# Kernel tuning notes

Measured on AMD Instinct MI355X. Metric: run time of the kernel, lower is better.

## Reference

```python
import jax, jax.numpy as jnp
import numpy as np

B, T, C = 4, 2048, 1024
H, G = 16, 4            # n_head, n_groups (GQA)
D = C // H              # head_dim = 64
NEG_INF = -1e30


def setup_inputs() -> dict:
    key = jax.random.key(0)
    k1, k2, k3, k4 = jax.random.split(key, 4)
    x = jax.random.normal(k1, (B, T, C), dtype=jnp.float32)
    Wq = jax.random.normal(k2, (C, C), dtype=jnp.float32) * 0.02
    Wkv = jax.random.normal(k3, (2 * G * D, C), dtype=jnp.float32) * 0.02
    Wproj = jax.random.normal(k4, (C, C), dtype=jnp.float32) * 0.02
    b_proj = jnp.zeros((C,), dtype=jnp.float32)
    return {"x": x, "Wq": Wq, "Wkv": Wkv, "Wproj": Wproj, "b_proj": b_proj}


def reference(x, Wq, Wkv, Wproj, b_proj):
    # q projection: [B,T,C] -> [B,H,T,D]
    q = (x @ Wq.T).reshape(B, T, H, D).transpose(0, 2, 1, 3)
    # fused kv projection -> split into k,v each [B,G,T,D]
    kv = x @ Wkv.T
    k = kv[..., : G * D].reshape(B, T, G, D).transpose(0, 2, 1, 3)
    v = kv[..., G * D :].reshape(B, T, G, D).transpose(0, 2, 1, 3)
    # torch .repeat tiles groups: head h uses kv group h % G
    k = jnp.tile(k, (1, H // G, 1, 1))  # [B,H,T,D]
    v = jnp.tile(v, (1, H // G, 1, 1))
    scale = 1.0 / jnp.sqrt(jnp.asarray(D, dtype=x.dtype))
    scores = jnp.einsum("bhqd,bhkd->bhqk", q, k) * scale  # [B,H,T,T]
    causal = jnp.tril(jnp.ones((T, T), dtype=bool))
    scores = jnp.where(causal, scores, NEG_INF)
    att = jax.nn.softmax(scores, axis=-1)
    y = jnp.einsum("bhqk,bhkd->bhqd", att, v)  # [B,H,T,D]
    y = y.transpose(0, 2, 1, 3).reshape(B, T, C)
    return y @ Wproj.T + b_proj
```

## Files before the change

### kernel.cpp

```cpp
#include <hip/hip_runtime.h>
#include <math.h>
#include <stdint.h>

#define B_ 4
#define T_ 2048
#define C_ 1024
#define H_ 16
#define G_ 4
#define D_ 64
#define KVC_ 512

typedef unsigned short u16;
typedef short bf16x8 __attribute__((ext_vector_type(8)));
typedef float f32x4 __attribute__((ext_vector_type(4)));

__device__ __forceinline__ u16 f2bf(float f) {
  uint32_t u = __builtin_bit_cast(uint32_t, f);
  u += 0x7fffu + ((u >> 16) & 1u);
  return (u16)(u >> 16);
}

__device__ __forceinline__ void gload16(const void* g, void* l) {
  __builtin_amdgcn_global_load_lds((const __attribute__((address_space(1))) void*)g,
                                   (__attribute__((address_space(3))) void*)l, 16, 0, 0);
}

__global__ __launch_bounds__(256)
void cvt_bf16(const float* __restrict__ s, u16* __restrict__ d, int n4, float scale) {
  int i = blockIdx.x * 256 + threadIdx.x;
  const int stride = gridDim.x * 256;
  for (; i < n4; i += stride) {
    const float4 v = ((const float4*)s)[i];
    uint2 o;
    o.x = (uint32_t)f2bf(v.x * scale) | ((uint32_t)f2bf(v.y * scale) << 16);
    o.y = (uint32_t)f2bf(v.z * scale) | ((uint32_t)f2bf(v.w * scale) << 16);
    ((uint2*)d)[i] = o;
  }
}

template <int OUTF32>
__global__ __launch_bounds__(256)
void gemm_bf16(const u16* __restrict__ A, const u16* __restrict__ W,
               const float* __restrict__ bias, void* __restrict__ outp,
               int N, int K) {
  __shared__ __align__(16) u16 As[128 * 32];
  __shared__ __align__(16) u16 Ws[128 * 32];
  const int tid = threadIdx.x;
  const int l = tid & 63, w = tid >> 6;
  const int lhi = l >> 4, llo = l & 15;
  const int wr = w >> 1, wc = w & 1;
  const int m0 = blockIdx.x * 128, n0 = blockIdx.y * 128;

  const u16* a_src = A + (size_t)(m0 + 32 * w + (l >> 2)) * K + 8 * (l & 3);
  const u16* w_src = W + (size_t)(n0 + 32 * w + (l >> 2)) * K + 8 * (l & 3);
  u16* asl = As + 1024 * w;
  u16* wsl = Ws + 1024 * w;

  const f32x4 zero4 = {0.f, 0.f, 0.f, 0.f};
  f32x4 acc[4][4];
#pragma unroll
  for (int i = 0; i < 4; ++i)
#pragma unroll
    for (int j = 0; j < 4; ++j) acc[i][j] = zero4;

  for (int k0 = 0; k0 < K; k0 += 32) {
    __syncthreads();
    gload16(a_src + k0, asl);
    gload16(a_src + k0 + 16 * K, asl + 512);
    gload16(w_src + k0, wsl);
    gload16(w_src + k0 + 16 * K, wsl + 512);
    __syncthreads();
    bf16x8 af[4], wf[4];
#pragma unroll
    for (int mt = 0; mt < 4; ++mt)
      af[mt] = *(const bf16x8*)(As + (wr * 64 + mt * 16 + llo) * 32 + lhi * 8);
#pragma unroll
    for (int nt = 0; nt < 4; ++nt)
      wf[nt] = *(const bf16x8*)(Ws + (wc * 64 + nt * 16 + llo) * 32 + lhi * 8);
#pragma unroll
    for (int mt = 0; mt < 4; ++mt)
#pragma unroll
      for (int nt = 0; nt < 4; ++nt)
        acc[mt][nt] = __builtin_amdgcn_mfma_f32_16x16x32_bf16(af[mt], wf[nt], acc[mt][nt], 0, 0, 0);
  }

#pragma unroll
  for (int mt = 0; mt < 4; ++mt)
#pragma unroll
    for (int nt = 0; nt < 4; ++nt)
#pragma unroll
      for (int r = 0; r < 4; ++r) {
        const int row = m0 + wr * 64 + mt * 16 + 4 * lhi + r;
        const int col = n0 + wc * 64 + nt * 16 + llo;
        if (OUTF32)
          ((float*)outp)[(size_t)row * N + col] = acc[mt][nt][r] + bias[col];
        else
          ((u16*)outp)[(size_t)row * N + col] = f2bf(acc[mt][nt][r]);
      }
}

__global__ __launch_bounds__(256)
void attn_kernel(const u16* __restrict__ Qb, const u16* __restrict__ KVb,
                 u16* __restrict__ Yb) {
  const int qt = blockIdx.x;
  const int bh = blockIdx.y;
  const int b = bh >> 4, h = bh & 15, g = h & (G_ - 1);
  const int tid = threadIdx.x;
  const int l = tid & 63, w = tid >> 6;
  const int lhi = l >> 4, llo = l & 15, l7 = l & 7;

  __shared__ __align__(16) u16 Ks[64 * 64];
  __shared__ __align__(16) u16 Vt[64 * 64];
  __shared__ __align__(16) u16 Ps[4][16 * 64];

  const int q0 = qt * 64;
  const int qrow = q0 + 16 * w + llo;
  const u16* qptr = Qb + (size_t)(b * T_ + qrow) * C_ + h * D_ + 8 * lhi;
  const bf16x8 qf0 = *(const bf16x8*)(qptr);
  const bf16x8 qf1 = *(const bf16x8*)(qptr + 32);

  const f32x4 zero4 = {0.f, 0.f, 0.f, 0.f};
  f32x4 o[4];
#pragma unroll
  for (int i = 0; i < 4; ++i) o[i] = zero4;
  float m_s = -__builtin_inff();
  float l_s = 0.f;

  const int vkr = 2 * (tid >> 3);
  const int vdc = tid & 7;
  const int kr0s = 16 * w + (l >> 3);
  const int kcs = (l & 7);
  u16* ksl = Ks + 1024 * w;
  u16* Pw = Ps[w];
  const int rbase = 4 * lhi;

  for (int kt = 0; kt <= qt; ++kt) {
    const int kv0 = b * T_ + kt * 64;
    const u16* vsrc = KVb + (size_t)(kv0 + vkr) * KVC_ + G_ * D_ + g * D_ + 8 * vdc;
    const uint4 v0 = *(const uint4*)vsrc;
    const uint4 v1 = *(const uint4*)(vsrc + KVC_);

    __syncthreads();
    {
      const u16* ks0 = KVb + (size_t)(kv0 + kr0s) * KVC_ + g * D_ + 8 * (kcs ^ (kr0s & 7));
      gload16(ks0, ksl);
      gload16(ks0 + 8 * KVC_, ksl + 512);
    }
    {
      const u16* pv0 = (const u16*)&v0;
      const u16* pv1 = (const u16*)&v1;
#pragma unroll
      for (int i = 0; i < 8; ++i) {
        const int d = 8 * vdc + i;
        const uint32_t val = (uint32_t)pv0[i] | ((uint32_t)pv1[i] << 16);
        const int byte = d * 128 + (((vkr >> 3) ^ (d & 7)) << 4) + (vkr & 7) * 2;
        *(uint32_t*)((char*)Vt + byte) = val;
      }
    }
    __syncthreads();

    f32x4 st[4];
#pragma unroll
    for (int mt = 0; mt < 4; ++mt) st[mt] = zero4;
#pragma unroll
    for (int mt = 0; mt < 4; ++mt) {
      const int krow = 16 * mt + llo;
      const bf16x8 kf0 = *(const bf16x8*)(Ks + krow * 64 + (((lhi + 0) ^ l7) << 3));
      const bf16x8 kf1 = *(const bf16x8*)(Ks + krow * 64 + (((lhi + 4) ^ l7) << 3));
      st[mt] = __builtin_amdgcn_mfma_f32_16x16x32_bf16(kf0, qf0, st[mt], 0, 0, 0);
      st[mt] = __builtin_amdgcn_mfma_f32_16x16x32_bf16(kf1, qf1, st[mt], 0, 0, 0);
    }
    if (kt == qt) {
#pragma unroll
      for (int mt = 0; mt < 4; ++mt)
#pragma unroll
        for (int r = 0; r < 4; ++r) {
          const int kr_g = kt * 64 + 16 * mt + rbase + r;
          if (kr_g > qrow) st[mt][r] = -__builtin_inff();
        }
    }
    float mloc = -__builtin_inff();
#pragma unroll
    for (int mt = 0; mt < 4; ++mt)
#pragma unroll
      for (int r = 0; r < 4; ++r) mloc = fmaxf(mloc, st[mt][r]);
    mloc = fmaxf(mloc, __shfl_xor(mloc, 16));
    mloc = fmaxf(mloc, __shfl_xor(mloc, 32));
    const float mnew = fmaxf(m_s, mloc);
    const float corr = __expf(m_s - mnew);
    float p[4][4];
    float ls = 0.f;
#pragma unroll
    for (int mt = 0; mt < 4; ++mt)
#pragma unroll
      for (int r = 0; r < 4; ++r) {
        const float e = __expf(st[mt][r] - mnew);
        p[mt][r] = e;
        ls += e;
      }
    ls += __shfl_xor(ls, 16);
    ls += __shfl_xor(ls, 32);
    l_s = l_s * corr + ls;
    m_s = mnew;
    float c4[4];
#pragma unroll
    for (int r = 0; r < 4; ++r) c4[r] = __shfl(corr, rbase + r);
#pragma unroll
    for (int nt = 0; nt < 4; ++nt)
#pragma unroll
      for (int r = 0; r < 4; ++r) o[nt][r] *= c4[r];

#pragma unroll
    for (int mt = 0; mt < 4; ++mt)
#pragma unroll
      for (int pr = 0; pr < 2; ++pr) {
        const int kr0 = 16 * mt + rbase + 2 * pr;
        const uint32_t val =
            (uint32_t)f2bf(p[mt][2 * pr]) | ((uint32_t)f2bf(p[mt][2 * pr + 1]) << 16);
        const int byte = llo * 128 + (((kr0 >> 3) ^ l7) << 4) + (kr0 & 7) * 2;
        *(uint32_t*)((char*)Pw + byte) = val;
      }
#pragma unroll
    for (int ks = 0; ks < 2; ++ks) {
      const bf16x8 pf = *(const bf16x8*)(Pw + llo * 64 + (((lhi + 4 * ks) ^ l7) << 3));
#pragma unroll
      for (int nt = 0; nt < 4; ++nt) {
        const int d_l = 16 * nt + llo;
        const bf16x8 vf = *(const bf16x8*)(Vt + d_l * 64 + (((lhi + 4 * ks) ^ l7) << 3));
        o[nt] = __builtin_amdgcn_mfma_f32_16x16x32_bf16(pf, vf, o[nt], 0, 0, 0);
      }
    }
  }

  const float invl = 1.f / l_s;
  float i4[4];
#pragma unroll
  for (int r = 0; r < 4; ++r) i4[r] = __shfl(invl, rbase + r);
#pragma unroll
  for (int nt = 0; nt < 4; ++nt)
#pragma unroll
    for (int r = 0; r < 4; ++r) {
      const int qg = q0 + 16 * w + rbase + r;
      const int d = 16 * nt + llo;
      Yb[(size_t)(b * T_ + qg) * C_ + h * D_ + d] = f2bf(o[nt][r] * i4[r]);
    }
}

extern "C" void kernel_launch(void* const* d_in, const int* in_sizes, int n_in,
                              void* d_out, int out_size, void* d_ws, size_t ws_size,
                              hipStream_t stream) {
  (void)in_sizes; (void)n_in; (void)out_size; (void)ws_size;
  const float* x     = (const float*)d_in[0];
  const float* Wq    = (const float*)d_in[1];
  const float* Wkv   = (const float*)d_in[2];
  const float* Wproj = (const float*)d_in[3];
  const float* bproj = (const float*)d_in[4];
  float* out = (float*)d_out;

  const size_t M = (size_t)B_ * T_;
  u16* xb   = (u16*)d_ws;
  u16* Qb   = xb + M * C_;
  u16* KVb  = Qb + M * C_;
  u16* wbuf = KVb + M * KVC_;
  u16* Yb   = xb;

  dim3 blk(256);
  cvt_bf16<<<2048, blk, 0, stream>>>(x, xb, (int)(M * C_ / 4), 1.f);
  cvt_bf16<<<512, blk, 0, stream>>>(Wq, wbuf, C_ * C_ / 4, 0.125f);
  gemm_bf16<0><<<dim3(64, 8), blk, 0, stream>>>(xb, wbuf, nullptr, Qb, C_, C_);
  cvt_bf16<<<256, blk, 0, stream>>>(Wkv, wbuf, KVC_ * C_ / 4, 1.f);
  gemm_bf16<0><<<dim3(64, 4), blk, 0, stream>>>(xb, wbuf, nullptr, KVb, KVC_, C_);
  attn_kernel<<<dim3(32, 64), blk, 0, stream>>>(Qb, KVb, Yb);
  cvt_bf16<<<512, blk, 0, stream>>>(Wproj, wbuf, C_ * C_ / 4, 1.f);
  gemm_bf16<1><<<dim3(64, 8), blk, 0, stream>>>(Yb, wbuf, bproj, out, C_, C_);
}
```

Baseline: 370.3 us.

## Fuse QKV GEMM, double-buffer K/V tiles, use 128-row attention blocks

Q and KV projections are merged into one GEMM over a concatenated bf16 weight staged temporarily in the output buffer, giving one launch and one shared read of x. The attention kernel now processes 128 query rows per 512-thread block, with warps skipping tiles fully above the diagonal. K/V tiles are double-buffered so the next tile's loads overlap current compute, which removes one barrier per iteration. Blocks are launched heaviest-first to balance the causal workload, and the V transpose swizzle is changed. These changes add LDS use and per-thread register pressure.

```diff
diff --git a/kernel.cpp b/kernel.cpp
--- a/kernel.cpp
+++ b/kernel.cpp
@@ -9,6 +9,9 @@
 #define G_ 4
 #define D_ 64
 #define KVC_ 512
+#define QKV_ 1536
+#define KOFF_ 1024
+#define VOFF_ 1280
 
 typedef unsigned short u16;
 typedef short bf16x8 __attribute__((ext_vector_type(8)));
@@ -99,23 +102,22 @@
       }
 }
 
-__global__ __launch_bounds__(256)
-void attn_kernel(const u16* __restrict__ Qb, const u16* __restrict__ KVb,
-                 u16* __restrict__ Yb) {
-  const int qt = blockIdx.x;
+__global__ __launch_bounds__(512)
+void attn_kernel(const u16* __restrict__ QKVb, u16* __restrict__ Yb) {
+  const int qtb = 15 - blockIdx.x;
   const int bh = blockIdx.y;
   const int b = bh >> 4, h = bh & 15, g = h & (G_ - 1);
   const int tid = threadIdx.x;
   const int l = tid & 63, w = tid >> 6;
   const int lhi = l >> 4, llo = l & 15, l7 = l & 7;
 
-  __shared__ __align__(16) u16 Ks[64 * 64];
-  __shared__ __align__(16) u16 Vt[64 * 64];
-  __shared__ __align__(16) u16 Ps[4][16 * 64];
-
-  const int q0 = qt * 64;
+  __shared__ __align__(16) u16 Ks[2][64 * 64];
+  __shared__ __align__(16) u16 Vt[2][64 * 64];
+  __shared__ __align__(16) u16 Ps[8][16 * 64];
+
+  const int q0 = qtb * 128;
   const int qrow = q0 + 16 * w + llo;
-  const u16* qptr = Qb + (size_t)(b * T_ + qrow) * C_ + h * D_ + 8 * lhi;
+  const u16* qptr = QKVb + (size_t)(b * T_ + qrow) * QKV_ + h * D_ + 8 * lhi;
   const bf16x8 qf0 = *(const bf16x8*)(qptr);
   const bf16x8 qf1 = *(const bf16x8*)(qptr + 32);
 
@@ -126,110 +128,136 @@
   float m_s = -__builtin_inff();
   float l_s = 0.f;
 
-  const int vkr = 2 * (tid >> 3);
-  const int vdc = tid & 7;
-  const int kr0s = 16 * w + (l >> 3);
-  const int kcs = (l & 7);
-  u16* ksl = Ks + 1024 * w;
+  const int skr = tid >> 3;
+  const int ksrc_off = 8 * ((tid & 7) ^ (skr & 7));
+  const int vkr = 2 * (tid >> 4);
+  const int vd4 = 4 * (tid & 15);
   u16* Pw = Ps[w];
   const int rbase = 4 * lhi;
-
-  for (int kt = 0; kt <= qt; ++kt) {
-    const int kv0 = b * T_ + kt * 64;
-    const u16* vsrc = KVb + (size_t)(kv0 + vkr) * KVC_ + G_ * D_ + g * D_ + 8 * vdc;
-    const uint4 v0 = *(const uint4*)vsrc;
-    const uint4 v1 = *(const uint4*)(vsrc + KVC_);
-
+  const int qmax_w = q0 + 16 * w + 15;
+  const int ntiles = 2 * qtb + 2;
+
+  {
+    const int kv0 = b * T_;
+    gload16(QKVb + (size_t)(kv0 + skr) * QKV_ + KOFF_ + g * D_ + ksrc_off,
+            Ks[0] + 512 * w);
+    const u16* vsrc = QKVb + (size_t)(kv0 + vkr) * QKV_ + VOFF_ + g * D_ + vd4;
+    const uint2 a = *(const uint2*)vsrc;
+    const uint2 c = *(const uint2*)(vsrc + QKV_);
+    const u16* p0 = (const u16*)&a;
+    const u16* p1 = (const u16*)&c;
+#pragma unroll
+    for (int i = 0; i < 4; ++i) {
+      const int d = vd4 + i;
+      const uint32_t val = (uint32_t)p0[i] | ((uint32_t)p1[i] << 16);
+      const int p = (vkr >> 3) ^ (d & 7) ^ ((d >> 3) & 7);
+      *(uint32_t*)((char*)Vt[0] + d * 128 + (p << 4) + (vkr & 7) * 2) = val;
+    }
+  }
+  __syncthreads();
+
+  int cur = 0;
+  for (int kt = 0; kt < ntiles; ++kt) {
+    const bool have_next = (kt + 1) < ntiles;
+    uint2 vr0, vr1;
+    if (have_next) {
+      const int kv0n = b * T_ + (kt + 1) * 64;
+      gload16(QKVb + (size_t)(kv0n + skr) * QKV_ + KOFF_ + g * D_ + ksrc_off,
+              Ks[cur ^ 1] + 512 * w);
+      const u16* vsrc = QKVb + (size_t)(kv0n + vkr) * QKV_ + VOFF_ + g * D_ + vd4;
+      vr0 = *(const uint2*)vsrc;
+      vr1 = *(const uint2*)(vsrc + QKV_);
+    }
+
+    if (kt * 64 <= qmax_w) {
+      f32x4 st[4];
+#pragma unroll
+      for (int mt = 0; mt < 4; ++mt) st[mt] = zero4;
+#pragma unroll
+      for (int mt = 0; mt < 4; ++mt) {
+        const int krow = 16 * mt + llo;
+        const u16* kb = Ks[cur] + krow * 64;
+        const bf16x8 kf0 = *(const bf16x8*)(kb + ((lhi ^ l7) << 3));
+        const bf16x8 kf1 = *(const bf16x8*)(kb + (((lhi + 4) ^ l7) << 3));
+        st[mt] = __builtin_amdgcn_mfma_f32_16x16x32_bf16(kf0, qf0, st[mt], 0, 0, 0);
+        st[mt] = __builtin_amdgcn_mfma_f32_16x16x32_bf16(kf1, qf1, st[mt], 0, 0, 0);
+      }
+      if (kt * 64 + 63 > q0 + 16 * w) {
+#pragma unroll
+        for (int mt = 0; mt < 4; ++mt)
+#pragma unroll
+          for (int r = 0; r < 4; ++r) {
+            const int kr_g = kt * 64 + 16 * mt + rbase + r;
+            if (kr_g > qrow) st[mt][r] = -__builtin_inff();
+          }
+      }
+      float mloc = -__builtin_inff();
+#pragma unroll
+      for (int mt = 0; mt < 4; ++mt)
+#pragma unroll
+        for (int r = 0; r < 4; ++r) mloc = fmaxf(mloc, st[mt][r]);
+      mloc = fmaxf(mloc, __shfl_xor(mloc, 16));
+      mloc = fmaxf(mloc, __shfl_xor(mloc, 32));
+      const float mnew = fmaxf(m_s, mloc);
+      const float corr = __expf(m_s - mnew);
+      float ls = 0.f;
+#pragma unroll
+      for (int mt = 0; mt < 4; ++mt)
+#pragma unroll
+        for (int r = 0; r < 4; ++r) {
+          const float e = __expf(st[mt][r] - mnew);
+          st[mt][r] = e;
+          ls += e;
+        }
+      ls += __shfl_xor(ls, 16);
+      ls += __shfl_xor(ls, 32);
+      l_s = l_s * corr + ls;
+      m_s = mnew;
+      float c4[4];
+#pragma unroll
+      for (int r = 0; r < 4; ++r) c4[r] = __shfl(corr, rbase + r);
+#pragma unroll
+      for (int nt = 0; nt < 4; ++nt)
+#pragma unroll
+        for (int r = 0; r < 4; ++r) o[nt][r] *= c4[r];
+
+#pragma unroll
+      for (int mt = 0; mt < 4; ++mt)
+#pragma unroll
+        for (int pr = 0; pr < 2; ++pr) {
+          const int kr0 = 16 * mt + rbase + 2 * pr;
+          const uint32_t val = (uint32_t)f2bf(st[mt][2 * pr]) |
+                               ((uint32_t)f2bf(st[mt][2 * pr + 1]) << 16);
+          *(uint32_t*)((char*)Pw + llo * 128 + (((kr0 >> 3) ^ l7) << 4) +
+                       (kr0 & 7) * 2) = val;
+        }
+#pragma unroll
+      for (int ks = 0; ks < 2; ++ks) {
+        const bf16x8 pf = *(const bf16x8*)(Pw + llo * 64 + (((lhi + 4 * ks) ^ l7) << 3));
+#pragma unroll
+        for (int nt = 0; nt < 4; ++nt) {
+          const int d_l = 16 * nt + llo;
+          const int fd = l7 ^ ((2 * nt + (llo >> 3)) & 7);
+          const bf16x8 vf = *(const bf16x8*)(Vt[cur] + d_l * 64 +
+                                             (((lhi + 4 * ks) ^ fd) << 3));
+          o[nt] = __builtin_amdgcn_mfma_f32_16x16x32_bf16(pf, vf, o[nt], 0, 0, 0);
+        }
+      }
+    }
+
+    if (have_next) {
+      const u16* p0 = (const u16*)&vr0;
+      const u16* p1 = (const u16*)&vr1;
+#pragma unroll
+      for (int i = 0; i < 4; ++i) {
+        const int d = vd4 + i;
+        const uint32_t val = (uint32_t)p0[i] | ((uint32_t)p1[i] << 16);
+        const int p = (vkr >> 3) ^ (d & 7) ^ ((d >> 3) & 7);
+        *(uint32_t*)((char*)Vt[cur ^ 1] + d * 128 + (p << 4) + (vkr & 7) * 2) = val;
+      }
+    }
     __syncthreads();
-    {
-      const u16* ks0 = KVb + (size_t)(kv0 + kr0s) * KVC_ + g * D_ + 8 * (kcs ^ (kr0s & 7));
-      gload16(ks0, ksl);
-      gload16(ks0 + 8 * KVC_, ksl + 512);
-    }
-    {
-      const u16* pv0 = (const u16*)&v0;
-      const u16* pv1 = (const u16*)&v1;
-#pragma unroll
-      for (int i = 0; i < 8; ++i) {
-        const int d = 8 * vdc + i;
-        const uint32_t val = (uint32_t)pv0[i] | ((uint32_t)pv1[i] << 16);
-        const int byte = d * 128 + (((vkr >> 3) ^ (d & 7)) << 4) + (vkr & 7) * 2;
-        *(uint32_t*)((char*)Vt + byte) = val;
-      }
-    }
-    __syncthreads();
-
-    f32x4 st[4];
-#pragma unroll
-    for (int mt = 0; mt < 4; ++mt) st[mt] = zero4;
-#pragma unroll
-    for (int mt = 0; mt < 4; ++mt) {
-      const int krow = 16 * mt + llo;
-      const bf16x8 kf0 = *(const bf16x8*)(Ks + krow * 64 + (((lhi + 0) ^ l7) << 3));
-      const bf16x8 kf1 = *(const bf16x8*)(Ks + krow * 64 + (((lhi + 4) ^ l7) << 3));
-      st[mt] = __builtin_amdgcn_mfma_f32_16x16x32_bf16(kf0, qf0, st[mt], 0, 0, 0);
-      st[mt] = __builtin_amdgcn_mfma_f32_16x16x32_bf16(kf1, qf1, st[mt], 0, 0, 0);
-    }
-    if (kt == qt) {
-#pragma unroll
-      for (int mt = 0; mt < 4; ++mt)
-#pragma unroll
-        for (int r = 0; r < 4; ++r) {
-          const int kr_g = kt * 64 + 16 * mt + rbase + r;
-          if (kr_g > qrow) st[mt][r] = -__builtin_inff();
-        }
-    }
-    float mloc = -__builtin_inff();
-#pragma unroll
-    for (int mt = 0; mt < 4; ++mt)
-#pragma unroll
-      for (int r = 0; r < 4; ++r) mloc = fmaxf(mloc, st[mt][r]);
-    mloc = fmaxf(mloc, __shfl_xor(mloc, 16));
-    mloc = fmaxf(mloc, __shfl_xor(mloc, 32));
-    const float mnew = fmaxf(m_s, mloc);
-    const float corr = __expf(m_s - mnew);
-    float p[4][4];
-    float ls = 0.f;
-#pragma unroll
-    for (int mt = 0; mt < 4; ++mt)
-#pragma unroll
-      for (int r = 0; r < 4; ++r) {
-        const float e = __expf(st[mt][r] - mnew);
-        p[mt][r] = e;
-        ls += e;
-      }
-    ls += __shfl_xor(ls, 16);
-    ls += __shfl_xor(ls, 32);
-    l_s = l_s * corr + ls;
-    m_s = mnew;
-    float c4[4];
-#pragma unroll
-    for (int r = 0; r < 4; ++r) c4[r] = __shfl(corr, rbase + r);
-#pragma unroll
-    for (int nt = 0; nt < 4; ++nt)
-#pragma unroll
-      for (int r = 0; r < 4; ++r) o[nt][r] *= c4[r];
-
-#pragma unroll
-    for (int mt = 0; mt < 4; ++mt)
-#pragma unroll
-      for (int pr = 0; pr < 2; ++pr) {
-        const int kr0 = 16 * mt + rbase + 2 * pr;
-        const uint32_t val =
-            (uint32_t)f2bf(p[mt][2 * pr]) | ((uint32_t)f2bf(p[mt][2 * pr + 1]) << 16);
-        const int byte = llo * 128 + (((kr0 >> 3) ^ l7) << 4) + (kr0 & 7) * 2;
-        *(uint32_t*)((char*)Pw + byte) = val;
-      }
-#pragma unroll
-    for (int ks = 0; ks < 2; ++ks) {
-      const bf16x8 pf = *(const bf16x8*)(Pw + llo * 64 + (((lhi + 4 * ks) ^ l7) << 3));
-#pragma unroll
-      for (int nt = 0; nt < 4; ++nt) {
-        const int d_l = 16 * nt + llo;
-        const bf16x8 vf = *(const bf16x8*)(Vt + d_l * 64 + (((lhi + 4 * ks) ^ l7) << 3));
-        o[nt] = __builtin_amdgcn_mfma_f32_16x16x32_bf16(pf, vf, o[nt], 0, 0, 0);
-      }
-    }
+    cur ^= 1;
   }
 
   const float invl = 1.f / l_s;
@@ -258,19 +286,18 @@
   float* out = (float*)d_out;
 
   const size_t M = (size_t)B_ * T_;
-  u16* xb   = (u16*)d_ws;
-  u16* Qb   = xb + M * C_;
-  u16* KVb  = Qb + M * C_;
-  u16* wbuf = KVb + M * KVC_;
-  u16* Yb   = xb;
+  u16* xb    = (u16*)d_ws;
+  u16* QKVb  = xb + M * C_;
+  u16* wpb   = QKVb + M * QKV_;
+  u16* wqkv  = (u16*)d_out;
+  u16* Yb    = xb;
 
   dim3 blk(256);
   cvt_bf16<<<2048, blk, 0, stream>>>(x, xb, (int)(M * C_ / 4), 1.f);
-  cvt_bf16<<<512, blk, 0, stream>>>(Wq, wbuf, C_ * C_ / 4, 0.125f);
-  gemm_bf16<0><<<dim3(64, 8), blk, 0, stream>>>(xb, wbuf, nullptr, Qb, C_, C_);
-  cvt_bf16<<<256, blk, 0, stream>>>(Wkv, wbuf, KVC_ * C_ / 4, 1.f);
-  gemm_bf16<0><<<dim3(64, 4), blk, 0, stream>>>(xb, wbuf, nullptr, KVb, KVC_, C_);
-  attn_kernel<<<dim3(32, 64), blk, 0, stream>>>(Qb, KVb, Yb);
-  cvt_bf16<<<512, blk, 0, stream>>>(Wproj, wbuf, C_ * C_ / 4, 1.f);
-  gemm_bf16<1><<<dim3(64, 8), blk, 0, stream>>>(Yb, wbuf, bproj, out, C_, C_);
-}
+  cvt_bf16<<<512, blk, 0, stream>>>(Wq, wqkv, C_ * C_ / 4, 0.125f);
+  cvt_bf16<<<256, blk, 0, stream>>>(Wkv, wqkv + (size_t)C_ * C_, KVC_ * C_ / 4, 1.f);
+  gemm_bf16<0><<<dim3(64, 12), blk, 0, stream>>>(xb, wqkv, nullptr, QKVb, QKV_, C_);
+  attn_kernel<<<dim3(16, 64), dim3(512), 0, stream>>>(QKVb, Yb);
+  cvt_bf16<<<512, blk, 0, stream>>>(Wproj, wpb, C_ * C_ / 4, 1.f);
+  gemm_bf16<1><<<dim3(64, 8), blk, 0, stream>>>(Yb, wpb, bproj, out, C_, C_);
+}
```

After: 307.2 us. 1.21x faster.
